# Kernel optimization log

Measured on AMD Instinct MI355X. Metric: run time of the kernel, lower is better.

## Reference

```python
import jax, jax.numpy as jnp
from jax import lax
import numpy as np

H = 64          # featureDim (conv channels)
BN_EPS = 1e-5
COS_EPS = 1e-8


def _conv_block(x, w, b, g, beta):
    # Conv(k3, valid) + BatchNorm(batch stats, training mode) + ReLU + MaxPool2
    y = lax.conv_general_dilated(x, w, (1, 1), 'VALID',
                                 dimension_numbers=('NCHW', 'OIHW', 'NCHW'))
    y = y + b[None, :, None, None]
    mu = jnp.mean(y, axis=(0, 2, 3), keepdims=True)
    var = jnp.var(y, axis=(0, 2, 3), keepdims=True)
    y = (y - mu) * lax.rsqrt(var + BN_EPS) * g[None, :, None, None] + beta[None, :, None, None]
    y = jax.nn.relu(y)
    return lax.reduce_window(y, -jnp.inf, lax.max, (1, 1, 2, 2), (1, 1, 2, 2), 'VALID')


def _lstm_dir(xs, Wi, Wh, bi, bh, h, c):
    # one direction of nn.LSTM, batch size 1 (state vectors of shape [H])
    def step(carry, x):
        h, c = carry
        gates = x @ Wi.T + h @ Wh.T + bi + bh          # [4H], pytorch gate order i,f,g,o
        i_, f_, g_, o_ = jnp.split(gates, 4)
        c = jax.nn.sigmoid(f_) * c + jax.nn.sigmoid(i_) * jnp.tanh(g_)
        h = jax.nn.sigmoid(o_) * jnp.tanh(c)
        return (h, c), h
    _, hs = lax.scan(step, (h, c), xs)
    return hs  # [N, H]


def setup_inputs() -> dict:
    key = jax.random.key(0)
    ks = jax.random.split(key, 32)
    N, T, WAY = 1024, 1024, 20
    d = {}
    d['trainIm'] = jax.random.normal(ks[0], (N, 1, 28, 28), jnp.float32)
    d['trainLabel'] = jax.random.uniform(ks[1], (N, WAY), dtype=jnp.float32)
    d['testIm'] = jax.random.normal(ks[2], (T, 1, 28, 28), jnp.float32)
    d['testLabel'] = jax.random.uniform(ks[3], (T, WAY), dtype=jnp.float32)
    # featureNet params
    d['c1w'] = jax.random.normal(ks[4], (H, 1, 3, 3), jnp.float32) * 0.3
    d['c1b'] = jax.random.normal(ks[5], (H,), jnp.float32) * 0.05
    d['bn1g'] = jnp.ones((H,), jnp.float32)
    d['bn1b'] = jnp.zeros((H,), jnp.float32)
    d['c2w'] = jax.random.normal(ks[6], (H, H, 3, 3), jnp.float32) * 0.05
    d['c2b'] = jax.random.normal(ks[7], (H,), jnp.float32) * 0.05
    d['bn2g'] = jnp.ones((H,), jnp.float32)
    d['bn2b'] = jnp.zeros((H,), jnp.float32)
    d['c3w'] = jax.random.normal(ks[8], (H, H, 3, 3), jnp.float32) * 0.05
    d['c3b'] = jax.random.normal(ks[9], (H,), jnp.float32) * 0.05
    d['bn3g'] = jnp.ones((H,), jnp.float32)
    d['bn3b'] = jnp.zeros((H,), jnp.float32)
    # bidirectional nn.LSTM(H, H) params
    d['wi_f'] = jax.random.normal(ks[10], (4 * H, H), jnp.float32) * 0.1
    d['wh_f'] = jax.random.normal(ks[11], (4 * H, H), jnp.float32) * 0.1
    d['bi_f'] = jax.random.normal(ks[12], (4 * H,), jnp.float32) * 0.05
    d['bh_f'] = jax.random.normal(ks[13], (4 * H,), jnp.float32) * 0.05
    d['wi_b'] = jax.random.normal(ks[14], (4 * H, H), jnp.float32) * 0.1
    d['wh_b'] = jax.random.normal(ks[15], (4 * H, H), jnp.float32) * 0.1
    d['bi_b'] = jax.random.normal(ks[16], (4 * H,), jnp.float32) * 0.05
    d['bh_b'] = jax.random.normal(ks[17], (4 * H,), jnp.float32) * 0.05
    d['h0'] = jax.random.normal(ks[18], (2, 1, H), jnp.float32)
    d['c0'] = jax.random.normal(ks[19], (2, 1, H), jnp.float32)
    # AttenLSTMCell params + attLSTM initial state
    d['att_wih'] = jax.random.normal(ks[20], (H, 4 * H), jnp.float32) * 0.1
    d['att_whh'] = jax.random.normal(ks[21], (2 * H, 4 * H), jnp.float32) * 0.1
    d['att_b'] = jnp.zeros((4 * H,), jnp.float32)
    d['att_h0'] = jax.random.normal(ks[22], (1, H), jnp.float32)
    d['att_c0'] = jax.random.normal(ks[23], (1, H), jnp.float32)
    d['att_r0'] = jax.random.normal(ks[24], (1, H), jnp.float32)
    return d


def reference(trainIm, trainLabel, testIm, testLabel,
              c1w, c1b, bn1g, bn1b, c2w, c2b, bn2g, bn2b, c3w, c3b, bn3g, bn3b,
              wi_f, wh_f, bi_f, bh_f, wi_b, wh_b, bi_b, bh_b, h0, c0,
              att_wih, att_whh, att_b, att_h0, att_c0, att_r0):
    def feat(x):
        y = _conv_block(x, c1w, c1b, bn1g, bn1b)
        y = _conv_block(y, c2w, c2b, bn2g, bn2b)
        y = _conv_block(y, c3w, c3b, bn3g, bn3b)   # [B, 64, 1, 1]
        return y.reshape(-1, H)                    # [B, 64]

    ftr = feat(trainIm)   # [N, 64]
    fte = feat(testIm)    # [T, 64]

    # getCondEmbed_G: BiLSTM; cond[i] = fw[i] + bw_out[N-1-i] + x[i] == fw[i] + bw_raw[i] + x[i]
    hf = _lstm_dir(ftr, wi_f, wh_f, bi_f, bh_f, h0[0, 0], c0[0, 0])
    hb_raw = _lstm_dir(ftr[::-1], wi_b, wh_b, bi_b, bh_b, h0[1, 0], c0[1, 0])
    cond_train = hf + hb_raw + ftr                 # [N, 64]

    # getCondEmbed_F: sequential attLSTM over test samples (state persists across samples)
    def att_step(carry, x):
        h, c, r = carry                            # each [64]
        hcat = jnp.concatenate([h, r])             # [128]
        gates = hcat @ att_whh + x @ att_wih + att_b   # [256], cell gate order f,i,o,g
        f_, i_, o_, g_ = jnp.split(gates, 4)
        c = jax.nn.sigmoid(f_) * c + jax.nn.sigmoid(i_) * jnp.tanh(g_)
        h = jax.nn.sigmoid(o_) * jnp.tanh(c) + x   # residual add of testF
        att = jax.nn.softmax(cond_train @ h)       # [N] attention over support set
        r = att @ cond_train                       # [64] read vector
        return (h, c, r), h

    _, cond_test = lax.scan(att_step, (att_h0[0], att_c0[0], att_r0[0]), fte)  # [T, 64]

    # getLabel: cosine-similarity softmax attention over support labels
    num = cond_test @ cond_train.T                                       # [T, N]
    den = jnp.linalg.norm(cond_test, axis=1)[:, None] * jnp.linalg.norm(cond_train, axis=1)[None, :]
    sim = num / jnp.maximum(den, COS_EPS)
    att = jax.nn.softmax(sim, axis=1)
    return att @ trainLabel                                              # [T, way]
```

## Files before the change

### kernel.cpp

```cpp
#include <hip/hip_runtime.h>
#include <stdint.h>

__device__ __forceinline__ float bf2f(uint16_t v){ return __uint_as_float(((uint32_t)v) << 16); }
__device__ __forceinline__ uint16_t f2bf(float x){
  uint32_t u = __float_as_uint(x);
  return (uint16_t)((u + 0x7fffu + ((u >> 16) & 1u)) >> 16);
}
__device__ __forceinline__ float sigf(float x){
  float cx = fminf(fmaxf(x, -88.f), 88.f);
  return 1.f/(1.f + expf(-cx));
}
__device__ __forceinline__ float tanh_s(float x){
  float cx = fminf(fmaxf(x, -44.f), 44.f);
  return tanhf(cx);
}
__device__ __forceinline__ float fast_sig(float x){
  float cx = fminf(fmaxf(x, -60.f), 60.f);
  return 1.f/(1.f + __expf(-cx));
}
__device__ __forceinline__ float fast_tanh(float x){
  float cx = fminf(fmaxf(x, -15.f), 15.f);
  float e = __expf(2.f*cx);
  return (e - 1.f)/(e + 1.f);
}

static const size_t OFF_STATS = 0;
static const size_t OFF_FLAG  = 3072;
static const size_t OFF_AB    = 4096;
static const size_t OFF_P2R   = 8192;
static const size_t OFF_Y3    = 13115392;
static const size_t OFF_F     = 17833984;
static const size_t OFF_XI    = 18358272;
static const size_t OFF_XATT  = 20455424;
static const size_t OFF_CA    = 21504000;
static const size_t OFF_CB    = 21766144;
static const size_t OFF_COND  = 22028288;
static const size_t OFF_NC    = 22290432;
static const size_t OFF_CT    = 22294528;

__global__ void k_sniff(const uint32_t* im, float* stats, int* flag){
  int t = threadIdx.x;
  for (int i = t; i < 768; i += 256) stats[i] = 0.f;
  if (t < 64){
    uint32_t w = im[t];
    uint32_t e = (w >> 7) & 0xffu;
    bool sane = (e >= 100u && e <= 140u);
    unsigned long long m = __ballot(sane);
    if (t == 0) flag[0] = (__popcll(m) < 48) ? 1 : 0;
  }
}

__global__ __launch_bounds__(256) void k_conv1_stats(const void* im0, const void* im1,
        const void* w1, const void* b1, float* stats, const int* flag){
  __shared__ float xs[784];
  __shared__ float wl[576];
  __shared__ float bl1[64];
  __shared__ float rs[256], rq[256];
  int img = blockIdx.x;
  bool f32 = flag[0] != 0;
  if (f32){
    const float* im = (img < 1024) ? ((const float*)im0 + img*784) : ((const float*)im1 + (img-1024)*784);
    for (int i = threadIdx.x; i < 784; i += 256) xs[i] = im[i];
    for (int i = threadIdx.x; i < 576; i += 256) wl[i] = ((const float*)w1)[i];
    if (threadIdx.x < 64) bl1[threadIdx.x] = ((const float*)b1)[threadIdx.x];
  } else {
    const uint16_t* im = (img < 1024) ? ((const uint16_t*)im0 + img*784) : ((const uint16_t*)im1 + (img-1024)*784);
    for (int i = threadIdx.x; i < 784; i += 256) xs[i] = bf2f(im[i]);
    for (int i = threadIdx.x; i < 576; i += 256) wl[i] = bf2f(((const uint16_t*)w1)[i]);
    if (threadIdx.x < 64) bl1[threadIdx.x] = bf2f(((const uint16_t*)b1)[threadIdx.x]);
  }
  __syncthreads();
  int c = threadIdx.x & 63, pg = threadIdx.x >> 6;
  float w[9];
  #pragma unroll
  for (int k = 0; k < 9; k++) w[k] = wl[c*9+k];
  float bias = bl1[c];
  float s = 0.f, q = 0.f;
  for (int pos = pg; pos < 676; pos += 4){
    int y = pos/26, x = pos - y*26;
    const float* p = xs + y*28 + x;
    float acc = bias;
    #pragma unroll
    for (int dy = 0; dy < 3; dy++)
      #pragma unroll
      for (int dx = 0; dx < 3; dx++)
        acc += w[dy*3+dx]*p[dy*28+dx];
    s += acc; q += acc*acc;
  }
  rs[threadIdx.x] = s; rq[threadIdx.x] = q;
  __syncthreads();
  if (threadIdx.x < 64){
    float S = rs[c] + rs[c+64] + rs[c+128] + rs[c+192];
    float Q = rq[c] + rq[c+64] + rq[c+128] + rq[c+192];
    int batch = img >> 10;
    atomicAdd(&stats[batch*128 + c*2 + 0], S);
    atomicAdd(&stats[batch*128 + c*2 + 1], Q);
  }
}

__global__ void k_bnfin(const float* stats, float* ab, const void* g, const void* be,
                        int layer, float invc, const int* flag){
  __shared__ float gl[64], bel[64];
  int t = threadIdx.x;
  bool f32 = flag[0] != 0;
  if (t < 64){
    if (f32){ gl[t] = ((const float*)g)[t]; bel[t] = ((const float*)be)[t]; }
    else    { gl[t] = bf2f(((const uint16_t*)g)[t]); bel[t] = bf2f(((const uint16_t*)be)[t]); }
  }
  __syncthreads();
  if (t >= 128) return;
  int batch = t >> 6, c = t & 63;
  float s = stats[layer*256 + batch*128 + c*2];
  float q = stats[layer*256 + batch*128 + c*2 + 1];
  float mu = s*invc;
  float var = fmaxf(q*invc - mu*mu, 0.f);
  float A = gl[c] * rsqrtf(var + 1e-5f);
  float B = bel[c] - mu*A;
  ab[layer*256 + batch*128 + c*2]     = A;
  ab[layer*256 + batch*128 + c*2 + 1] = B;
}

__global__ __launch_bounds__(256) void k_conv2(const void* im0, const void* im1,
        const void* w1, const void* b1, const float* ab,
        const void* w2, const void* c2b, float* p2raw, float* stats, const int* flag){
  __shared__ float img[10816];
  __shared__ float ovl[4608];
  __shared__ float cbias[64];
  int b = blockIdx.x;
  int tid = threadIdx.x;
  bool f32 = flag[0] != 0;
  if (f32){
    const float* im = (b < 1024) ? ((const float*)im0 + b*784) : ((const float*)im1 + (b-1024)*784);
    for (int i = tid; i < 784; i += 256) ovl[i] = im[i];
    for (int i = tid; i < 576; i += 256) ovl[784+i] = ((const float*)w1)[i];
    if (tid < 64){ ovl[1360+tid] = ((const float*)b1)[tid]; cbias[tid] = ((const float*)c2b)[tid]; }
  } else {
    const uint16_t* im = (b < 1024) ? ((const uint16_t*)im0 + b*784) : ((const uint16_t*)im1 + (b-1024)*784);
    for (int i = tid; i < 784; i += 256) ovl[i] = bf2f(im[i]);
    for (int i = tid; i < 576; i += 256) ovl[784+i] = bf2f(((const uint16_t*)w1)[i]);
    if (tid < 64){ ovl[1360+tid] = bf2f(((const uint16_t*)b1)[tid]); cbias[tid] = bf2f(((const uint16_t*)c2b)[tid]); }
  }
  __syncthreads();
  int c = tid & 63, pg = tid >> 6;
  int batch = b >> 10;
  {
    float w[9];
    #pragma unroll
    for (int k = 0; k < 9; k++) w[k] = ovl[784 + c*9 + k];
    float bias = ovl[1360 + c];
    float A = ab[batch*128 + c*2], B = ab[batch*128 + c*2 + 1];
    for (int pp = pg; pp < 169; pp += 4){
      int py = pp/13, px = pp - py*13;
      float m = 0.f;
      #pragma unroll
      for (int q = 0; q < 4; q++){
        int yy = 2*py + (q>>1), xx = 2*px + (q&1);
        const float* p = ovl + yy*28 + xx;
        float acc = bias;
        #pragma unroll
        for (int dy = 0; dy < 3; dy++)
          #pragma unroll
          for (int dx = 0; dx < 3; dx++)
            acc += w[dy*3+dx]*p[dy*28+dx];
        m = fmaxf(m, A*acc + B);
      }
      img[c*169 + pp] = m;
    }
  }
  int lane = tid & 63, wv = tid >> 6;
  int pos0 = lane;
  int pos1 = lane + 64;
  bool v1 = (pos1 < 121);
  int p1c = v1 ? pos1 : pos0;
  int y0 = pos0/11, x0 = pos0 - y0*11;
  int y1 = p1c/11,  x1 = p1c - y1*11;
  float acc0[16], acc1[16];
  #pragma unroll
  for (int cc = 0; cc < 16; cc++){ acc0[cc]=0.f; acc1[cc]=0.f; }
  for (int ch = 0; ch < 8; ch++){
    int ci0 = ch*8;
    __syncthreads();
    if (f32){
      for (int i = tid; i < 4608; i += 256){
        int co = i/72, r = i - co*72;
        ovl[i] = ((const float*)w2)[(co*64 + ci0)*9 + r];
      }
    } else {
      for (int i = tid; i < 4608; i += 256){
        int co = i/72, r = i - co*72;
        ovl[i] = bf2f(((const uint16_t*)w2)[(co*64 + ci0)*9 + r]);
      }
    }
    __syncthreads();
    for (int cil = 0; cil < 8; cil++){
      int ci = ci0 + cil;
      float a[9], bv[9];
      const float* q0 = img + ci*169 + y0*13 + x0;
      const float* q1 = img + ci*169 + y1*13 + x1;
      #pragma unroll
      for (int dy = 0; dy < 3; dy++)
        #pragma unroll
        for (int dx = 0; dx < 3; dx++){
          a[dy*3+dx]  = q0[dy*13+dx];
          bv[dy*3+dx] = q1[dy*13+dx];
        }
      #pragma unroll
      for (int cc = 0; cc < 16; cc++){
        const float* wp = ovl + (wv*16+cc)*72 + cil*9;
        #pragma unroll
        for (int k = 0; k < 9; k++){
          acc0[cc] += wp[k]*a[k];
          acc1[cc] += wp[k]*bv[k];
        }
      }
    }
  }
  __syncthreads();
  float* ybuf = img;
  #pragma unroll
  for (int cc = 0; cc < 16; cc++){
    int co = wv*16 + cc;
    float bs = cbias[co];
    float u0 = acc0[cc] + bs;
    float u1 = acc1[cc] + bs;
    ybuf[co*121 + pos0] = u0;
    if (v1) ybuf[co*121 + pos1] = u1;
    float s = u0 + (v1 ? u1 : 0.f);
    float q = u0*u0 + (v1 ? u1*u1 : 0.f);
    #pragma unroll
    for (int off = 32; off; off >>= 1){
      s += __shfl_down(s, off);
      q += __shfl_down(q, off);
    }
    if (lane == 0){
      atomicAdd(&stats[256 + batch*128 + co*2 + 0], s);
      atomicAdd(&stats[256 + batch*128 + co*2 + 1], q);
    }
  }
  __syncthreads();
  for (int idx = tid; idx < 1600; idx += 256){
    int cc = idx/25, pp = idx - cc*25;
    int py = pp/5, px = pp - py*5;
    const float* s = ybuf + cc*121;
    float m = fmaxf(fmaxf(s[(2*py)*11 + 2*px], s[(2*py)*11 + 2*px + 1]),
                    fmaxf(s[(2*py+1)*11 + 2*px], s[(2*py+1)*11 + 2*px + 1]));
    p2raw[(size_t)b*1600 + idx] = m;
  }
}

__global__ __launch_bounds__(256) void k_conv3(const float* p2raw, const float* ab,
        const void* w3, const void* c3b, float* y3, float* stats, const int* flag){
  __shared__ float pimg[12800];
  __shared__ float wch[2304];
  __shared__ float cb3[64];
  __shared__ float abl[128];
  __shared__ float lstat[128];
  int b = blockIdx.x;
  int tid = threadIdx.x;
  bool f32 = flag[0] != 0;
  int batch = (b*8) >> 10;
  if (tid < 128){ abl[tid] = ab[256 + batch*128 + tid]; lstat[tid] = 0.f; }
  if (f32){ if (tid >= 128 && tid < 192) cb3[tid-128] = ((const float*)c3b)[tid-128]; }
  else    { if (tid >= 128 && tid < 192) cb3[tid-128] = bf2f(((const uint16_t*)c3b)[tid-128]); }
  __syncthreads();
  for (int idx = tid; idx < 12800; idx += 256){
    int rem = idx & 1599;
    int cch = rem / 25;
    pimg[idx] = fmaxf(abl[cch*2]*p2raw[(size_t)b*12800 + idx] + abl[cch*2+1], 0.f);
  }
  int il = tid >> 5, sub = tid & 31;
  float acc[18];
  #pragma unroll
  for (int s = 0; s < 18; s++){
    int o = sub + s*32;
    acc[s] = cb3[o/9];
  }
  for (int ch = 0; ch < 16; ch++){
    int ci0 = ch*4;
    __syncthreads();
    if (f32){
      for (int i = tid; i < 2304; i += 256){
        int co = i/36, r = i - co*36;
        wch[i] = ((const float*)w3)[(co*64 + ci0)*9 + r];
      }
    } else {
      for (int i = tid; i < 2304; i += 256){
        int co = i/36, r = i - co*36;
        wch[i] = bf2f(((const uint16_t*)w3)[(co*64 + ci0)*9 + r]);
      }
    }
    __syncthreads();
    #pragma unroll
    for (int s = 0; s < 18; s++){
      int o = sub + s*32;
      int co = o/9, pos = o - co*9;
      int y = pos/3, x = pos - y*3;
      float a = acc[s];
      #pragma unroll
      for (int cil = 0; cil < 4; cil++){
        const float* p = pimg + il*1600 + (ci0+cil)*25 + y*5 + x;
        const float* w = wch + co*36 + cil*9;
        #pragma unroll
        for (int dy = 0; dy < 3; dy++)
          #pragma unroll
          for (int dx = 0; dx < 3; dx++)
            a += w[dy*3+dx]*p[dy*5+dx];
      }
      acc[s] = a;
    }
  }
  #pragma unroll
  for (int s = 0; s < 18; s++){
    int o = sub + s*32;
    int co = o/9;
    y3[(size_t)(b*8+il)*576 + o] = acc[s];
    atomicAdd(&lstat[co*2 + 0], acc[s]);
    atomicAdd(&lstat[co*2 + 1], acc[s]*acc[s]);
  }
  __syncthreads();
  if (tid < 128)
    atomicAdd(&stats[512 + batch*128 + tid], lstat[tid]);
}

__global__ __launch_bounds__(256) void k_pool3(const float* y3, const float* ab, float* ff){
  int idx = blockIdx.x*256 + threadIdx.x;
  int img = idx >> 6, c = idx & 63;
  int batch = img >> 10;
  float A = ab[512 + batch*128 + c*2], B = ab[512 + batch*128 + c*2 + 1];
  const float* p = y3 + (size_t)img*576 + c*9;
  float m = 0.f;
  m = fmaxf(m, A*p[0]+B);
  m = fmaxf(m, A*p[1]+B);
  m = fmaxf(m, A*p[3]+B);
  m = fmaxf(m, A*p[4]+B);
  ff[idx] = m;
}

__global__ __launch_bounds__(256) void k_xproj(const float* ff,
        const void* wi_f, const void* bi_f, const void* bh_f,
        const void* wi_b, const void* bi_b, const void* bh_b,
        const void* att_wih, const void* att_b,
        float* Xi, float* Xatt, const int* flag){
  int which = blockIdx.x >> 10, t = blockIdx.x & 1023;
  __shared__ float xv[64];
  bool f32 = flag[0] != 0;
  const float* row = (which == 0) ? ff + t*64
                   : (which == 1) ? ff + (1023 - t)*64
                   : ff + (1024 + t)*64;
  if (threadIdx.x < 64) xv[threadIdx.x] = row[threadIdx.x];
  __syncthreads();
  int j = threadIdx.x;
  if (which < 2){
    const void* wi = which ? wi_b : wi_f;
    const void* bi = which ? bi_b : bi_f;
    const void* bh = which ? bh_b : bh_f;
    float acc;
    if (f32){
      acc = ((const float*)bi)[j] + ((const float*)bh)[j];
      const float* wp = (const float*)wi + j*64;
      #pragma unroll 8
      for (int k = 0; k < 64; k++) acc += wp[k]*xv[k];
    } else {
      acc = bf2f(((const uint16_t*)bi)[j]) + bf2f(((const uint16_t*)bh)[j]);
      const uint16_t* wp = (const uint16_t*)wi + j*64;
      #pragma unroll 8
      for (int k = 0; k < 64; k++) acc += bf2f(wp[k])*xv[k];
    }
    Xi[(size_t)which*262144 + t*256 + j] = acc;
  } else {
    float acc;
    if (f32){
      acc = ((const float*)att_b)[j];
      for (int k = 0; k < 64; k++) acc += ((const float*)att_wih)[k*256 + j]*xv[k];
    } else {
      acc = bf2f(((const uint16_t*)att_b)[j]);
      for (int k = 0; k < 64; k++) acc += bf2f(((const uint16_t*)att_wih)[k*256 + j])*xv[k];
    }
    Xatt[t*256 + j] = acc;
  }
}

__global__ __launch_bounds__(256, 1) void k_bilstm(const void* wh_f, const void* wh_b,
        const void* h0, const void* c0, const float* Xi, float* condA, float* condB,
        const int* flag){
  int dir = blockIdx.x;
  int j = threadIdx.x;
  bool f32 = flag[0] != 0;
  float w[64];
  if (f32){
    const float* wp = (const float*)(dir ? wh_b : wh_f) + j*64;
    #pragma unroll
    for (int k = 0; k < 64; k++) w[k] = wp[k];
  } else {
    const uint16_t* wp = (const uint16_t*)(dir ? wh_b : wh_f) + j*64;
    #pragma unroll
    for (int k = 0; k < 64; k++) w[k] = bf2f(wp[k]);
  }
  __shared__ __align__(16) float h[64];
  __shared__ float ga[256];
  float c = 0.f;
  if (j < 64){
    if (f32){ h[j] = ((const float*)h0)[dir*64 + j]; c = ((const float*)c0)[dir*64 + j]; }
    else    { h[j] = bf2f(((const uint16_t*)h0)[dir*64 + j]); c = bf2f(((const uint16_t*)c0)[dir*64 + j]); }
  }
  __syncthreads();
  const float* X = Xi + (size_t)dir*262144;
  float* out = dir ? condB : condA;
  float xcur = X[j];
  for (int t = 0; t < 1024; t++){
    float xnext = (t < 1023) ? X[(t+1)*256 + j] : 0.f;
    float g0 = xcur, g1 = 0.f;
    #pragma unroll
    for (int k4 = 0; k4 < 16; k4 += 2){
      float4 ha = ((const float4*)h)[k4];
      float4 hb = ((const float4*)h)[k4+1];
      g0 += w[4*k4]*ha.x + w[4*k4+1]*ha.y + w[4*k4+2]*ha.z + w[4*k4+3]*ha.w;
      g1 += w[4*k4+4]*hb.x + w[4*k4+5]*hb.y + w[4*k4+6]*hb.z + w[4*k4+7]*hb.w;
    }
    float g = g0 + g1;
    ga[j] = (j < 128 || j >= 192) ? fast_sig(g) : fast_tanh(g);
    __syncthreads();
    if (j < 64){
      c = ga[64+j]*c + ga[j]*ga[128+j];
      float hv = ga[192+j]*fast_tanh(c);
      h[j] = hv;
      out[t*64 + j] = hv;
    }
    xcur = xnext;
    __syncthreads();
  }
}

__global__ void k_cond(const float* condA, const float* condB, const float* ff,
                       float* cond, float* ncond){
  int t = blockIdx.x, j = threadIdx.x;
  float v = condA[t*64+j] + condB[t*64+j] + ff[t*64+j];
  cond[t*64+j] = v;
  float s = v*v;
  #pragma unroll
  for (int off = 32; off; off >>= 1) s += __shfl_down(s, off);
  if (j == 0) ncond[t] = sqrtf(s);
}

__global__ __launch_bounds__(512, 1) void k_attlstm(
        const float* cond, const float* Xatt, const float* ff,
        const void* whh, const void* ah0, const void* ac0, const void* ar0,
        float* ctest, const int* flag){
  __shared__ float hr[128];
  __shared__ float gpart[512];
  __shared__ float pbuf[512*17];
  __shared__ float rs2[4][544];
  __shared__ float wred[16];
  int tid = threadIdx.x;
  bool f32 = flag[0] != 0;
  int j = tid & 255, half = tid >> 8;
  float wk[64];
  if (f32){
    const float* W = (const float*)whh + (size_t)half*64*256 + j;
    #pragma unroll
    for (int k = 0; k < 64; k++) wk[k] = W[k*256];
  } else {
    const uint16_t* W = (const uint16_t*)whh + (size_t)half*64*256 + j;
    #pragma unroll
    for (int k = 0; k < 64; k++) wk[k] = bf2f(W[k*256]);
  }
  float row0[64], row1[64];
  {
    const float4* r0 = (const float4*)(cond + (size_t)tid*64);
    const float4* r1 = (const float4*)(cond + (size_t)(tid+512)*64);
    #pragma unroll
    for (int k4 = 0; k4 < 16; k4++){
      float4 a = r0[k4]; float4 b = r1[k4];
      row0[4*k4]=a.x; row0[4*k4+1]=a.y; row0[4*k4+2]=a.z; row0[4*k4+3]=a.w;
      row1[4*k4]=b.x; row1[4*k4+1]=b.y; row1[4*k4+2]=b.z; row1[4*k4+3]=b.w;
    }
  }
  float c = 0.f;
  if (f32){
    if (tid < 64){ hr[tid] = ((const float*)ah0)[tid]; c = ((const float*)ac0)[tid]; }
    else if (tid < 128) hr[tid] = ((const float*)ar0)[tid-64];
  } else {
    if (tid < 64){ hr[tid] = bf2f(((const uint16_t*)ah0)[tid]); c = bf2f(((const uint16_t*)ac0)[tid]); }
    else if (tid < 128) hr[tid] = bf2f(((const uint16_t*)ar0)[tid-64]);
  }
  __syncthreads();
  int lane = tid & 63, wv = tid >> 6;
  const float* fte = ff + 65536;
  for (int st = 0; st < 1024; st++){
    float ga0 = (half == 0) ? Xatt[st*256 + j] : 0.f, ga1 = 0.f;
    {
      const float4* hc = (const float4*)(hr + half*64);
      #pragma unroll
      for (int k4 = 0; k4 < 16; k4 += 2){
        float4 hv = hc[k4];
        float4 hw = hc[k4+1];
        ga0 += wk[4*k4]*hv.x + wk[4*k4+1]*hv.y + wk[4*k4+2]*hv.z + wk[4*k4+3]*hv.w;
        ga1 += wk[4*k4+4]*hw.x + wk[4*k4+5]*hw.y + wk[4*k4+6]*hw.z + wk[4*k4+7]*hw.w;
      }
    }
    gpart[tid] = ga0 + ga1;
    __syncthreads();
    if (tid < 64){
      float xres = fte[st*64 + tid];
      float gf = gpart[tid]     + gpart[256+tid];
      float gi = gpart[64+tid]  + gpart[320+tid];
      float go = gpart[128+tid] + gpart[384+tid];
      float gg = gpart[192+tid] + gpart[448+tid];
      float f_ = fast_sig(gf), i_ = fast_sig(gi), o_ = fast_sig(go), g_ = fast_tanh(gg);
      c = f_*c + i_*g_;
      float hv = o_*fast_tanh(c) + xres;
      hr[tid] = hv;
      ctest[st*64 + tid] = hv;
    }
    __syncthreads();
    float lg0a = 0.f, lg0b = 0.f, lg1a = 0.f, lg1b = 0.f;
    {
      const float4* hq = (const float4*)hr;
      #pragma unroll
      for (int k4 = 0; k4 < 16; k4 += 2){
        float4 hv = hq[k4];
        float4 hw = hq[k4+1];
        lg0a += row0[4*k4]*hv.x + row0[4*k4+1]*hv.y + row0[4*k4+2]*hv.z + row0[4*k4+3]*hv.w;
        lg0b += row0[4*k4+4]*hw.x + row0[4*k4+5]*hw.y + row0[4*k4+6]*hw.z + row0[4*k4+7]*hw.w;
        lg1a += row1[4*k4]*hv.x + row1[4*k4+1]*hv.y + row1[4*k4+2]*hv.z + row1[4*k4+3]*hv.w;
        lg1b += row1[4*k4+4]*hw.x + row1[4*k4+5]*hw.y + row1[4*k4+6]*hw.z + row1[4*k4+7]*hw.w;
      }
    }
    float lg0 = lg0a + lg0b, lg1 = lg1a + lg1b;
    float mx = fmaxf(lg0, lg1);
    #pragma unroll
    for (int off = 32; off; off >>= 1) mx = fmaxf(mx, __shfl_xor(mx, off));
    if (lane == 0) wred[wv] = mx;
    __syncthreads();
    float gmax = fmaxf(fmaxf(fmaxf(wred[0],wred[1]),fmaxf(wred[2],wred[3])),
                       fmaxf(fmaxf(wred[4],wred[5]),fmaxf(wred[6],wred[7])));
    float e0 = __expf(lg0 - gmax), e1 = __expf(lg1 - gmax);
    float s = e0 + e1;
    #pragma unroll
    for (int off = 32; off; off >>= 1) s += __shfl_xor(s, off);
    if (lane == 0) wred[8+wv] = s;
    __syncthreads();
    float inv = 1.f/(((wred[8]+wred[9])+(wred[10]+wred[11]))
                   + ((wred[12]+wred[13])+(wred[14]+wred[15])));
    #pragma unroll
    for (int ch = 0; ch < 4; ch++){
      #pragma unroll
      for (int k = 0; k < 16; k++)
        pbuf[tid*17 + k] = e0*row0[ch*16+k] + e1*row1[ch*16+k];
      __syncthreads();
      {
        int kk = tid & 15, seg = tid >> 4;
        float a = 0.f;
        #pragma unroll
        for (int q = 0; q < 16; q++)
          a += pbuf[(seg*16+q)*17 + kk];
        rs2[ch][seg*17 + kk] = a;
      }
      __syncthreads();
    }
    if (tid < 64){
      int kk = lane & 15, chq = lane >> 4;
      float a = 0.f;
      #pragma unroll
      for (int sgm = 0; sgm < 32; sgm++) a += rs2[chq][sgm*17 + kk];
      hr[64 + lane] = a * inv;
    }
    __syncthreads();
  }
}

__global__ __launch_bounds__(256) void k_final(const float* ctest, const float* cond,
        const float* ncond, const void* labels, void* out, const int* flag){
  int t = blockIdx.x;
  __shared__ __align__(16) float q[64];
  __shared__ float sim[1024];
  __shared__ float red[4];
  __shared__ float accw[20];
  __shared__ float bcv[2];
  int tid = threadIdx.x;
  bool f32 = flag[0] != 0;
  if (tid < 64) q[tid] = ctest[t*64 + tid];
  if (tid < 20) accw[tid] = 0.f;
  __syncthreads();
  if (tid < 64){
    float s = q[tid]*q[tid];
    #pragma unroll
    for (int off = 32; off; off >>= 1) s += __shfl_down(s, off);
    if (tid == 0) bcv[0] = sqrtf(s);
  }
  __syncthreads();
  float nq = bcv[0];
  float mymax = -1e30f;
  for (int i = tid; i < 1024; i += 256){
    float d = 0.f;
    const float4* cr = (const float4*)(cond + i*64);
    #pragma unroll
    for (int k4 = 0; k4 < 16; k4++){
      float4 cv = cr[k4];
      float4 qv = ((const float4*)q)[k4];
      d += cv.x*qv.x + cv.y*qv.y + cv.z*qv.z + cv.w*qv.w;
    }
    float den = fmaxf(nq*ncond[i], 1e-8f);
    float sv = d/den;
    sim[i] = sv;
    mymax = fmaxf(mymax, sv);
  }
  int lane = tid & 63, wv = tid >> 6;
  #pragma unroll
  for (int off = 32; off; off >>= 1) mymax = fmaxf(mymax, __shfl_down(mymax, off));
  if (lane == 0) red[wv] = mymax;
  __syncthreads();
  if (tid == 0) bcv[1] = fmaxf(fmaxf(red[0], red[1]), fmaxf(red[2], red[3]));
  __syncthreads();
  float smax = bcv[1];
  float es = 0.f;
  float la[20];
  #pragma unroll
  for (int w = 0; w < 20; w++) la[w] = 0.f;
  if (f32){
    for (int i = tid; i < 1024; i += 256){
      float e = __expf(sim[i] - smax);
      es += e;
      const float* L = (const float*)labels + i*20;
      #pragma unroll
      for (int w = 0; w < 20; w++) la[w] += e*L[w];
    }
  } else {
    for (int i = tid; i < 1024; i += 256){
      float e = __expf(sim[i] - smax);
      es += e;
      const uint16_t* L = (const uint16_t*)labels + i*20;
      #pragma unroll
      for (int w = 0; w < 20; w++) la[w] += e*bf2f(L[w]);
    }
  }
  #pragma unroll
  for (int off = 32; off; off >>= 1) es += __shfl_down(es, off);
  if (lane == 0) red[wv] = es;
  #pragma unroll
  for (int w = 0; w < 20; w++) atomicAdd(&accw[w], la[w]);
  __syncthreads();
  if (tid == 0) bcv[0] = 1.f/(red[0] + red[1] + red[2] + red[3]);
  __syncthreads();
  if (tid < 20){
    float v = accw[tid]*bcv[0];
    if (f32) ((float*)out)[t*20 + tid] = v;
    else     ((uint16_t*)out)[t*20 + tid] = f2bf(v);
  }
}

extern "C" void kernel_launch(void* const* d_in, const int* in_sizes, int n_in,
                              void* d_out, int out_size, void* d_ws, size_t ws_size,
                              hipStream_t stream){
  const void* trainIm    = d_in[0];
  const void* trainLabel = d_in[1];
  const void* testIm     = d_in[2];
  const void* c1w  = d_in[4];
  const void* c1b  = d_in[5];
  const void* bn1g = d_in[6];
  const void* bn1b = d_in[7];
  const void* c2w  = d_in[8];
  const void* c2b  = d_in[9];
  const void* bn2g = d_in[10];
  const void* bn2b = d_in[11];
  const void* c3w  = d_in[12];
  const void* c3b  = d_in[13];
  const void* bn3g = d_in[14];
  const void* bn3b = d_in[15];
  const void* wi_f = d_in[16];
  const void* wh_f = d_in[17];
  const void* bi_f = d_in[18];
  const void* bh_f = d_in[19];
  const void* wi_b = d_in[20];
  const void* wh_b = d_in[21];
  const void* bi_b = d_in[22];
  const void* bh_b = d_in[23];
  const void* h0   = d_in[24];
  const void* c0   = d_in[25];
  const void* att_wih = d_in[26];
  const void* att_whh = d_in[27];
  const void* att_b   = d_in[28];
  const void* att_h0  = d_in[29];
  const void* att_c0  = d_in[30];
  const void* att_r0  = d_in[31];

  char* ws = (char*)d_ws;
  float* stats = (float*)(ws + OFF_STATS);
  int*   flag  = (int*)(ws + OFF_FLAG);
  float* ab    = (float*)(ws + OFF_AB);
  float* p2raw = (float*)(ws + OFF_P2R);
  float* y3    = (float*)(ws + OFF_Y3);
  float* ff    = (float*)(ws + OFF_F);
  float* Xi    = (float*)(ws + OFF_XI);
  float* Xatt  = (float*)(ws + OFF_XATT);
  float* condA = (float*)(ws + OFF_CA);
  float* condB = (float*)(ws + OFF_CB);
  float* cond  = (float*)(ws + OFF_COND);
  float* ncond = (float*)(ws + OFF_NC);
  float* ctest = (float*)(ws + OFF_CT);

  k_sniff<<<1, 256, 0, stream>>>((const uint32_t*)trainIm, stats, flag);
  k_conv1_stats<<<2048, 256, 0, stream>>>(trainIm, testIm, c1w, c1b, stats, flag);
  k_bnfin<<<1, 192, 0, stream>>>(stats, ab, bn1g, bn1b, 0, 1.f/692224.f, flag);
  k_conv2<<<2048, 256, 0, stream>>>(trainIm, testIm, c1w, c1b, ab, c2w, c2b, p2raw, stats, flag);
  k_bnfin<<<1, 192, 0, stream>>>(stats, ab, bn2g, bn2b, 1, 1.f/123904.f, flag);
  k_conv3<<<256, 256, 0, stream>>>(p2raw, ab, c3w, c3b, y3, stats, flag);
  k_bnfin<<<1, 192, 0, stream>>>(stats, ab, bn3g, bn3b, 2, 1.f/9216.f, flag);
  k_pool3<<<512, 256, 0, stream>>>(y3, ab, ff);
  k_xproj<<<3072, 256, 0, stream>>>(ff, wi_f, bi_f, bh_f, wi_b, bi_b, bh_b, att_wih, att_b, Xi, Xatt, flag);
  k_bilstm<<<2, 256, 0, stream>>>(wh_f, wh_b, h0, c0, Xi, condA, condB, flag);
  k_cond<<<1024, 64, 0, stream>>>(condA, condB, ff, cond, ncond);
  k_attlstm<<<1, 512, 0, stream>>>(cond, Xatt, ff, att_whh, att_h0, att_c0, att_r0, ctest, flag);
  k_final<<<1024, 256, 0, stream>>>(ctest, cond, ncond, trainLabel, d_out, flag);
}
```

Baseline: 5.997 ms.

## Split bidirectional LSTM recurrence across two thread halves per gate

The recurrent BiLSTM kernel now runs 512 threads per direction, with each gate's 64-term hidden dot product split into two 32-term halves. The halves are summed through shared memory before the activations are applied. This shortens the per-step serial dot product and halves the weight registers per thread, at the cost of an extra barrier and a shared-memory reduction every timestep. The attention LSTM kernel also gets explicit work-group-size and waves-per-EU attributes in place of its launch bounds, which may change its register allocation.

After: 6.074 ms. Within noise of the previous version (+1.3%).

```diff
diff --git a/kernel.cpp b/kernel.cpp
--- a/kernel.cpp
+++ b/kernel.cpp
@@ -380,51 +380,61 @@
   }
 }
 
-__global__ __launch_bounds__(256, 1) void k_bilstm(const void* wh_f, const void* wh_b,
+__global__ __attribute__((amdgpu_flat_work_group_size(512,512)))
+void k_bilstm(const void* wh_f, const void* wh_b,
         const void* h0, const void* c0, const float* Xi, float* condA, float* condB,
         const int* flag){
   int dir = blockIdx.x;
-  int j = threadIdx.x;
+  int tid = threadIdx.x;
+  int j = tid & 255, half = tid >> 8;
   bool f32 = flag[0] != 0;
-  float w[64];
+  float w[32];
   if (f32){
-    const float* wp = (const float*)(dir ? wh_b : wh_f) + j*64;
-    #pragma unroll
-    for (int k = 0; k < 64; k++) w[k] = wp[k];
+    const float* wp = (const float*)(dir ? wh_b : wh_f) + j*64 + half*32;
+    #pragma unroll
+    for (int k = 0; k < 32; k++) w[k] = wp[k];
   } else {
-    const uint16_t* wp = (const uint16_t*)(dir ? wh_b : wh_f) + j*64;
-    #pragma unroll
-    for (int k = 0; k < 64; k++) w[k] = bf2f(wp[k]);
+    const uint16_t* wp = (const uint16_t*)(dir ? wh_b : wh_f) + j*64 + half*32;
+    #pragma unroll
+    for (int k = 0; k < 32; k++) w[k] = bf2f(wp[k]);
   }
   __shared__ __align__(16) float h[64];
+  __shared__ float gpart[512];
   __shared__ float ga[256];
   float c = 0.f;
-  if (j < 64){
-    if (f32){ h[j] = ((const float*)h0)[dir*64 + j]; c = ((const float*)c0)[dir*64 + j]; }
-    else    { h[j] = bf2f(((const uint16_t*)h0)[dir*64 + j]); c = bf2f(((const uint16_t*)c0)[dir*64 + j]); }
+  if (tid < 64){
+    if (f32){ h[tid] = ((const float*)h0)[dir*64 + tid]; c = ((const float*)c0)[dir*64 + tid]; }
+    else    { h[tid] = bf2f(((const uint16_t*)h0)[dir*64 + tid]); c = bf2f(((const uint16_t*)c0)[dir*64 + tid]); }
   }
   __syncthreads();
   const float* X = Xi + (size_t)dir*262144;
   float* out = dir ? condB : condA;
-  float xcur = X[j];
+  float xcur = (half == 0) ? X[j] : 0.f;
   for (int t = 0; t < 1024; t++){
-    float xnext = (t < 1023) ? X[(t+1)*256 + j] : 0.f;
+    float xnext = (half == 0 && t < 1023) ? X[(t+1)*256 + j] : 0.f;
     float g0 = xcur, g1 = 0.f;
-    #pragma unroll
-    for (int k4 = 0; k4 < 16; k4 += 2){
-      float4 ha = ((const float4*)h)[k4];
-      float4 hb = ((const float4*)h)[k4+1];
-      g0 += w[4*k4]*ha.x + w[4*k4+1]*ha.y + w[4*k4+2]*ha.z + w[4*k4+3]*ha.w;
-      g1 += w[4*k4+4]*hb.x + w[4*k4+5]*hb.y + w[4*k4+6]*hb.z + w[4*k4+7]*hb.w;
-    }
-    float g = g0 + g1;
-    ga[j] = (j < 128 || j >= 192) ? fast_sig(g) : fast_tanh(g);
-    __syncthreads();
-    if (j < 64){
-      c = ga[64+j]*c + ga[j]*ga[128+j];
-      float hv = ga[192+j]*fast_tanh(c);
-      h[j] = hv;
-      out[t*64 + j] = hv;
+    {
+      const float4* hp = (const float4*)(h + half*32);
+      #pragma unroll
+      for (int k4 = 0; k4 < 8; k4 += 2){
+        float4 ha = hp[k4];
+        float4 hb = hp[k4+1];
+        g0 += w[4*k4]*ha.x + w[4*k4+1]*ha.y + w[4*k4+2]*ha.z + w[4*k4+3]*ha.w;
+        g1 += w[4*k4+4]*hb.x + w[4*k4+5]*hb.y + w[4*k4+6]*hb.z + w[4*k4+7]*hb.w;
+      }
+    }
+    gpart[tid] = g0 + g1;
+    __syncthreads();
+    if (tid < 256){
+      float g = gpart[tid] + gpart[tid + 256];
+      ga[tid] = (tid < 128 || tid >= 192) ? fast_sig(g) : fast_tanh(g);
+    }
+    __syncthreads();
+    if (tid < 64){
+      c = ga[64+tid]*c + ga[tid]*ga[128+tid];
+      float hv = ga[192+tid]*fast_tanh(c);
+      h[tid] = hv;
+      out[t*64 + tid] = hv;
     }
     xcur = xnext;
     __syncthreads();
@@ -442,7 +452,8 @@
   if (j == 0) ncond[t] = sqrtf(s);
 }
 
-__global__ __launch_bounds__(512, 1) void k_attlstm(
+__global__ __attribute__((amdgpu_flat_work_group_size(512,512), amdgpu_waves_per_eu(2,2)))
+void k_attlstm(
         const float* cond, const float* Xatt, const float* ff,
         const void* whh, const void* ah0, const void* ac0, const void* ar0,
         float* ctest, const int* flag){
@@ -708,7 +719,7 @@
   k_bnfin<<<1, 192, 0, stream>>>(stats, ab, bn3g, bn3b, 2, 1.f/9216.f, flag);
   k_pool3<<<512, 256, 0, stream>>>(y3, ab, ff);
   k_xproj<<<3072, 256, 0, stream>>>(ff, wi_f, bi_f, bh_f, wi_b, bi_b, bh_b, att_wih, att_b, Xi, Xatt, flag);
-  k_bilstm<<<2, 256, 0, stream>>>(wh_f, wh_b, h0, c0, Xi, condA, condB, flag);
+  k_bilstm<<<2, 512, 0, stream>>>(wh_f, wh_b, h0, c0, Xi, condA, condB, flag);
   k_cond<<<1024, 64, 0, stream>>>(condA, condB, ff, cond, ncond);
   k_attlstm<<<1, 512, 0, stream>>>(cond, Xatt, ff, att_whh, att_h0, att_c0, att_r0, ctest, flag);
   k_final<<<1024, 256, 0, stream>>>(ctest, cond, ncond, trainLabel, d_out, flag);
```
